# Performance work log

Measured on AMD Instinct MI355X. Metric: run time of the kernel, lower is better.

## Reference

```python
import jax, jax.numpy as jnp
import numpy as np

D_MODEL = 512
N_HEAD = 8


def setup_inputs() -> dict:
    key = jax.random.key(0)
    ks = jax.random.split(key, 9)
    s = 1.0 / np.sqrt(D_MODEL)
    inp = {
        "x": jax.random.normal(ks[0], (2, 4096, D_MODEL), dtype=jnp.float32),
        "wq": jax.random.uniform(ks[1], (D_MODEL, D_MODEL), jnp.float32, -s, s),
        "bq": jax.random.uniform(ks[2], (D_MODEL,), jnp.float32, -s, s),
        "wk": jax.random.uniform(ks[3], (D_MODEL, D_MODEL), jnp.float32, -s, s),
        "bk": jax.random.uniform(ks[4], (D_MODEL,), jnp.float32, -s, s),
        "wv": jax.random.uniform(ks[5], (D_MODEL, D_MODEL), jnp.float32, -s, s),
        "bv": jax.random.uniform(ks[6], (D_MODEL,), jnp.float32, -s, s),
        "wo": jax.random.uniform(ks[7], (D_MODEL, D_MODEL), jnp.float32, -s, s),
        "bo": jax.random.uniform(ks[8], (D_MODEL,), jnp.float32, -s, s),
    }
    return inp


def reference(x, wq, bq, wk, bk, wv, bv, wo, bo):
    B, S, D = x.shape
    H = N_HEAD
    Dh = D // H

    def split_heads(t):  # [B,S,D] -> [B,H,S,Dh]
        return t.reshape(B, S, H, Dh).transpose(0, 2, 1, 3)

    q = split_heads(x @ wq.T + bq)
    k = split_heads(x @ wk.T + bk)
    v = split_heads(x @ wv.T + bv)

    # explicit (unfused) attention, matching the torch module
    score = jnp.einsum("bhsd,bhtd->bhst", q, k) / jnp.sqrt(jnp.float32(Dh))
    attn = jax.nn.softmax(score, axis=-1)
    out = jnp.einsum("bhst,bhtd->bhsd", attn, v)  # [B,H,S,Dh]

    out = out.transpose(0, 2, 1, 3).reshape(B, S, D)
    return out @ wo.T + bo
```

## Files before the change

kernel.cpp:

```cpp
#include <hip/hip_runtime.h>
#include <math.h>

#define S_LEN 4096
#define DMODEL 512
#define NHEAD 8
#define E_ELEMS ((size_t)8192 * 512)
#define QSCALE 0.18033688f

typedef __attribute__((ext_vector_type(8))) short bf16x8;
typedef __attribute__((ext_vector_type(4))) float f32x4;
typedef __attribute__((ext_vector_type(16))) float f32x16;
typedef unsigned short u16;
typedef unsigned int u32;

__device__ __forceinline__ u16 f2bf(float f) {
    u32 u = __float_as_uint(f);
    u += 0x7FFFu + ((u >> 16) & 1u);
    return (u16)(u >> 16);
}

#define MFMA16(a, b, c) __builtin_amdgcn_mfma_f32_16x16x32_bf16((a), (b), (c), 0, 0, 0)
#define MFMA32(a, b, c) __builtin_amdgcn_mfma_f32_32x32x16_bf16((a), (b), (c), 0, 0, 0)

__global__ __launch_bounds__(256) void cvt_x(const float* __restrict__ in,
                                             u16* __restrict__ out, int n4) {
    const int i = blockIdx.x * 256 + threadIdx.x;
    if (i >= n4) return;
    const float4 v = ((const float4*)in)[i];
    uint2 hp;
    hp.x = (u32)f2bf(v.x) | ((u32)f2bf(v.y) << 16);
    hp.y = (u32)f2bf(v.z) | ((u32)f2bf(v.w) << 16);
    ((uint2*)out)[i] = hp;
}

__global__ __launch_bounds__(256) void cvt_w(
    const float* __restrict__ wq, const float* __restrict__ wk,
    const float* __restrict__ wv, const float* __restrict__ wo,
    u16* __restrict__ oq, u16* __restrict__ ok,
    u16* __restrict__ ov, u16* __restrict__ oo) {
    const int i = blockIdx.x * 256 + threadIdx.x;
    {
        const float4 v = ((const float4*)wq)[i];
        uint2 hp;
        hp.x = (u32)f2bf(v.x * QSCALE) | ((u32)f2bf(v.y * QSCALE) << 16);
        hp.y = (u32)f2bf(v.z * QSCALE) | ((u32)f2bf(v.w * QSCALE) << 16);
        ((uint2*)oq)[i] = hp;
    }
    {
        const float4 v = ((const float4*)wk)[i];
        uint2 hp;
        hp.x = (u32)f2bf(v.x) | ((u32)f2bf(v.y) << 16);
        hp.y = (u32)f2bf(v.z) | ((u32)f2bf(v.w) << 16);
        ((uint2*)ok)[i] = hp;
    }
    {
        const float4 v = ((const float4*)wv)[i];
        uint2 hp;
        hp.x = (u32)f2bf(v.x) | ((u32)f2bf(v.y) << 16);
        hp.y = (u32)f2bf(v.z) | ((u32)f2bf(v.w) << 16);
        ((uint2*)ov)[i] = hp;
    }
    {
        const float4 v = ((const float4*)wo)[i];
        uint2 hp;
        hp.x = (u32)f2bf(v.x) | ((u32)f2bf(v.y) << 16);
        hp.y = (u32)f2bf(v.z) | ((u32)f2bf(v.w) << 16);
        ((uint2*)oo)[i] = hp;
    }
}

template<int MODE>
__global__ __launch_bounds__(256) void proj2_kernel(
    const u16* __restrict__ Abf,
    const u16* __restrict__ W0, const float* __restrict__ Bi0,
    const u16* __restrict__ W1, const float* __restrict__ Bi1,
    u16* __restrict__ Qo, u16* __restrict__ Ko, float* __restrict__ Out)
{
    __shared__ __align__(16) u16 sm[16384];
    u16* As = sm;
    u16* Bs = sm + 8192;

    const int tid = threadIdx.x;
    const int w = tid >> 6, l = tid & 63, g = (l >> 4), c = l & 15;
    const int wr = w >> 1, wc = w & 1;
    const int bm = blockIdx.x * 128;
    const int n0 = blockIdx.y * 128;
    const int z = (MODE == 0) ? blockIdx.z : 0;
    const u16* W   = z ? W1 : W0;
    const float* Bi = z ? Bi1 : Bi0;
    const float bsc = (MODE == 0 && z == 0) ? QSCALE : 1.0f;

    const int sr = l >> 3;
    const int slot = l & 7;

    f32x4 acc[4][4];
    #pragma unroll
    for (int i = 0; i < 4; ++i)
        #pragma unroll
        for (int j = 0; j < 4; ++j) acc[i][j] = (f32x4){0.f, 0.f, 0.f, 0.f};

    #pragma unroll 1
    for (int kt = 0; kt < 8; ++kt) {
        const int k0 = kt * 64;
        __syncthreads();
        #pragma unroll
        for (int i = 0; i < 4; ++i) {
            const int row = i * 32 + w * 8 + sr;
            const int scol = (slot ^ (row & 7)) * 8;
            __builtin_amdgcn_global_load_lds(
                Abf + (size_t)(bm + row) * DMODEL + k0 + scol,
                As + (i * 32 + w * 8) * 64, 16, 0, 0);
            __builtin_amdgcn_global_load_lds(
                W + (size_t)(n0 + row) * DMODEL + k0 + scol,
                Bs + (i * 32 + w * 8) * 64, 16, 0, 0);
        }
        __syncthreads();

        #pragma unroll
        for (int kc = 0; kc < 2; ++kc) {
            bf16x8 a[4], b[4];
            #pragma unroll
            for (int mf = 0; mf < 4; ++mf) {
                const int ra = wr * 64 + mf * 16 + c;
                a[mf] = *(const bf16x8*)(As + ra * 64 + (((kc * 4 + g) ^ (ra & 7)) * 8));
            }
            #pragma unroll
            for (int nf = 0; nf < 4; ++nf) {
                const int rb = wc * 64 + nf * 16 + c;
                b[nf] = *(const bf16x8*)(Bs + rb * 64 + (((kc * 4 + g) ^ (rb & 7)) * 8));
            }
            #pragma unroll
            for (int mf = 0; mf < 4; ++mf)
                #pragma unroll
                for (int nf = 0; nf < 4; ++nf)
                    acc[mf][nf] = MFMA16(a[mf], b[nf], acc[mf][nf]);
        }
    }

    #pragma unroll
    for (int mf = 0; mf < 4; ++mf)
        #pragma unroll
        for (int nf = 0; nf < 4; ++nf) {
            const int n = n0 + wc * 64 + nf * 16 + c;
            const float bias = Bi[n] * bsc;
            #pragma unroll
            for (int r = 0; r < 4; ++r) {
                const int m = bm + wr * 64 + mf * 16 + 4 * g + r;
                const float v = acc[mf][nf][r] + bias;
                if (MODE == 1) {
                    Out[(size_t)m * DMODEL + n] = v;
                } else {
                    const int b = m >> 12, s = m & (S_LEN - 1);
                    const int hh = n >> 6, dd = n & 63;
                    const size_t o = ((size_t)((b * NHEAD + hh) * S_LEN + s)) * 64 + dd;
                    if (z == 0) Qo[o] = f2bf(v);
                    else        Ko[o] = f2bf(v);
                }
            }
        }
}

__global__ __launch_bounds__(256) void proj_v_kernel(
    const u16* __restrict__ Abf, const u16* __restrict__ Wv,
    const float* __restrict__ Bv, u16* __restrict__ Vt)
{
    __shared__ __align__(16) u16 sm[18432];
    u16* Ah = sm;
    u16* Bh = sm + 9216;

    const int tid = threadIdx.x;
    const int w = tid >> 6, lane = tid & 63, g = lane >> 4, c = lane & 15;
    const int bm = blockIdx.x * 128;
    const int n0 = blockIdx.y * 64;

    f32x4 acc[2][4];
    #pragma unroll
    for (int a = 0; a < 2; ++a)
        #pragma unroll
        for (int b = 0; b < 4; ++b) acc[a][b] = (f32x4){0.f, 0.f, 0.f, 0.f};

    #pragma unroll 1
    for (int kt = 0; kt < 8; ++kt) {
        const int k0 = kt * 64;
        __syncthreads();
        #pragma unroll
        for (int i = 0; i < 4; ++i) {
            const int slot = i * 256 + tid;
            const int r = slot >> 3, c8 = slot & 7;
            *(uint4*)(Ah + r * 72 + c8 * 8) =
                *(const uint4*)(Abf + (size_t)(bm + r) * DMODEL + k0 + c8 * 8);
        }
        #pragma unroll
        for (int i = 0; i < 2; ++i) {
            const int slot = i * 256 + tid;
            const int r = slot >> 3, c8 = slot & 7;
            *(uint4*)(Bh + r * 72 + c8 * 8) =
                *(const uint4*)(Wv + (size_t)(n0 + r) * DMODEL + k0 + c8 * 8);
        }
        __syncthreads();

        #pragma unroll
        for (int kc = 0; kc < 2; ++kc) {
            bf16x8 a[2], b[4];
            #pragma unroll
            for (int mf = 0; mf < 2; ++mf)
                a[mf] = *(const bf16x8*)(Ah + (w * 32 + mf * 16 + c) * 72 + kc * 32 + g * 8);
            #pragma unroll
            for (int nf = 0; nf < 4; ++nf)
                b[nf] = *(const bf16x8*)(Bh + (nf * 16 + c) * 72 + kc * 32 + g * 8);
            #pragma unroll
            for (int mf = 0; mf < 2; ++mf)
                #pragma unroll
                for (int nf = 0; nf < 4; ++nf)
                    acc[mf][nf] = MFMA16(a[mf], b[nf], acc[mf][nf]);
        }
    }

    __syncthreads();
    float* scr = (float*)sm;
    #pragma unroll
    for (int mf = 0; mf < 2; ++mf)
        #pragma unroll
        for (int nf = 0; nf < 4; ++nf) {
            const float bias = Bv[n0 + nf * 16 + c];
            #pragma unroll
            for (int r = 0; r < 4; ++r)
                scr[(w * 32 + mf * 16 + 4 * g + r) * 72 + nf * 16 + c] =
                    acc[mf][nf][r] + bias;
        }
    __syncthreads();
    const int d = tid & 63, sb = tid >> 6;
    const int b = bm >> 12, h = n0 >> 6;
    const size_t obase =
        ((size_t)((b * NHEAD + h) * 64 + d)) * S_LEN + (bm & (S_LEN - 1)) + sb * 32;
    u16 th[32];
    #pragma unroll
    for (int j = 0; j < 32; ++j)
        th[j] = f2bf(scr[(sb * 32 + j) * 72 + d]);
    #pragma unroll
    for (int q = 0; q < 4; ++q)
        *(uint4*)(Vt + obase + q * 8) = *(const uint4*)&th[q * 8];
}

__global__ __launch_bounds__(512, 4) void attn_kernel(
    const u16* __restrict__ Qb, const u16* __restrict__ Kb,
    const u16* __restrict__ Vt, u16* __restrict__ AO)
{
    __shared__ __align__(16) u16 sm[32768];

    const int tid = threadIdx.x;
    const int w = tid >> 6, l = tid & 63;
    const int kvg = w >> 2, wq = w & 3;
    const int r0 = l & 31, hi = l >> 5;

    const int f = blockIdx.x;
    const int wg = (f & 7) * 64 + (f >> 3);
    const int bh = wg >> 5, qb = wg & 31;
    const int b = bh >> 3, h = bh & 7;

    const size_t hoff = (size_t)bh * S_LEN * 64;
    const int qw = qb * 128 + wq * 32;
    const int kv0 = kvg * 2048;

    bf16x8 qf[4];
    #pragma unroll
    for (int kc = 0; kc < 4; ++kc)
        qf[kc] = *(const bf16x8*)(Qb + hoff + (size_t)(qw + r0) * 64 + kc * 16 + hi * 8);

    const int rbase = r0 * 64;
    int soff[4];
    #pragma unroll
    for (int j = 0; j < 4; ++j) soff[j] = ((2 * j + hi) ^ (r0 & 7)) * 8;

    const int srow0 = wq * 16 + (l >> 3);
    const int slot  = l & 7;
    const int srow1 = srow0 + 8;
    const u16* srcK0 = Kb + hoff + (size_t)(kv0 + srow0) * 64 + ((slot ^ (srow0 & 7)) * 8);
    const u16* srcK1 = Kb + hoff + (size_t)(kv0 + srow1) * 64 + ((slot ^ (srow1 & 7)) * 8);
    const u16* srcV0 = Vt + ((size_t)bh * 64 + srow0) * S_LEN + kv0 + ((slot ^ (srow0 & 7)) * 8);
    const u16* srcV1 = Vt + ((size_t)bh * 64 + srow1) * S_LEN + kv0 + ((slot ^ (srow1 & 7)) * 8);

    u16* const grp = sm + kvg * 16384;

#define STAGE(bufb, t) do {                                                        \
        u16* kb_ = grp + (bufb) * 8192 + wq * 1024;                                \
        u16* vb_ = kb_ + 4096;                                                     \
        __builtin_amdgcn_global_load_lds(srcK0 + (size_t)(t) * 4096, kb_,       16, 0, 0); \
        __builtin_amdgcn_global_load_lds(srcK1 + (size_t)(t) * 4096, kb_ + 512, 16, 0, 0); \
        __builtin_amdgcn_global_load_lds(srcV0 + (size_t)(t) * 64,   vb_,       16, 0, 0); \
        __builtin_amdgcn_global_load_lds(srcV1 + (size_t)(t) * 64,   vb_ + 512, 16, 0, 0); \
    } while (0)

    f32x16 o0 = {0.f,0.f,0.f,0.f,0.f,0.f,0.f,0.f,0.f,0.f,0.f,0.f,0.f,0.f,0.f,0.f};
    f32x16 o1 = {0.f,0.f,0.f,0.f,0.f,0.f,0.f,0.f,0.f,0.f,0.f,0.f,0.f,0.f,0.f,0.f};
    f32x16 lacc = {0.f,0.f,0.f,0.f,0.f,0.f,0.f,0.f,0.f,0.f,0.f,0.f,0.f,0.f,0.f,0.f};

    STAGE(0, 0);
    __syncthreads();
    int buf = 0;

    #pragma unroll 1
    for (int t = 0; t < 32; ++t) {
        if (t + 1 < 32) STAGE(buf ^ 1, t + 1);

        const u16* Kb_s = grp + buf * 8192;
        const u16* Vb_s = Kb_s + 4096;

        f32x16 s0 = {0.f,0.f,0.f,0.f,0.f,0.f,0.f,0.f,0.f,0.f,0.f,0.f,0.f,0.f,0.f,0.f};
        f32x16 s1 = {0.f,0.f,0.f,0.f,0.f,0.f,0.f,0.f,0.f,0.f,0.f,0.f,0.f,0.f,0.f,0.f};
        __builtin_amdgcn_s_setprio(1);
        #pragma unroll
        for (int kc = 0; kc < 4; ++kc) {
            const bf16x8 k0 = *(const bf16x8*)(Kb_s + rbase + soff[kc]);
            const bf16x8 k1 = *(const bf16x8*)(Kb_s + 2048 + rbase + soff[kc]);
            s0 = MFMA32(k0, qf[kc], s0);
            s1 = MFMA32(k1, qf[kc], s1);
        }
        __builtin_amdgcn_s_setprio(0);

        bf16x8 pa[4];
        #pragma unroll
        for (int kvf = 0; kvf < 2; ++kvf) {
            f32x16 pex;
            #pragma unroll
            for (int r = 0; r < 16; ++r)
                pex[r] = __builtin_amdgcn_exp2f(kvf ? s1[r] : s0[r]);
            lacc += pex;
            #pragma unroll
            for (int hf = 0; hf < 2; ++hf) {
                const int rb = hf * 8;
                u32 x0, y0, x1, y1;
                asm("v_cvt_pk_bf16_f32 %0, %1, %2" : "=v"(x0) : "v"(pex[rb+0]), "v"(pex[rb+1]));
                asm("v_cvt_pk_bf16_f32 %0, %1, %2" : "=v"(y0) : "v"(pex[rb+4]), "v"(pex[rb+5]));
                asm("v_cvt_pk_bf16_f32 %0, %1, %2" : "=v"(x1) : "v"(pex[rb+2]), "v"(pex[rb+3]));
                asm("v_cvt_pk_bf16_f32 %0, %1, %2" : "=v"(y1) : "v"(pex[rb+6]), "v"(pex[rb+7]));
                asm volatile("v_permlane32_swap_b32 %0, %1" : "+v"(x0), "+v"(y0));
                asm volatile("v_permlane32_swap_b32 %0, %1" : "+v"(x1), "+v"(y1));
                union { u32 u[4]; bf16x8 v; } P;
                P.u[0] = x0; P.u[1] = x1; P.u[2] = y0; P.u[3] = y1;
                pa[kvf * 2 + hf] = P.v;
            }
        }

        __builtin_amdgcn_s_setprio(1);
        #pragma unroll
        for (int kvc = 0; kvc < 4; ++kvc) {
            const bf16x8 v0 = *(const bf16x8*)(Vb_s + rbase + soff[kvc]);
            const bf16x8 v1 = *(const bf16x8*)(Vb_s + 2048 + rbase + soff[kvc]);
            o0 = MFMA32(pa[kvc], v0, o0);
            o1 = MFMA32(pa[kvc], v1, o1);
        }
        __builtin_amdgcn_s_setprio(0);

        __syncthreads();
        buf ^= 1;
    }
#undef STAGE

    float lsum = 0.f;
    #pragma unroll
    for (int r = 0; r < 16; ++r) lsum += lacc[r];
    lsum += __shfl_xor(lsum, 32);

    float* scrF = (float*)sm;
    float* Lsh  = scrF + 8192;
    if (hi == 0) Lsh[w * 32 + r0] = lsum;
    if (kvg == 1) {
        #pragma unroll
        for (int r = 0; r < 16; ++r) {
            const int q = (r & 3) + 8 * (r >> 2) + 4 * hi;
            scrF[wq * 2048 + q * 64 + r0]      = o0[r];
            scrF[wq * 2048 + q * 64 + 32 + r0] = o1[r];
        }
    }
    __syncthreads();
    if (kvg == 0) {
        #pragma unroll
        for (int r = 0; r < 16; ++r) {
            const int q = (r & 3) + 8 * (r >> 2) + 4 * hi;
            const float L = Lsh[wq * 32 + q] + Lsh[(wq + 4) * 32 + q];
            const float inv = 1.0f / L;
            const int s = qw + q;
            const size_t base = ((size_t)b * S_LEN + s) * DMODEL + h * 64;
            AO[base + r0]      = f2bf((o0[r] + scrF[wq * 2048 + q * 64 + r0])      * inv);
            AO[base + 32 + r0] = f2bf((o1[r] + scrF[wq * 2048 + q * 64 + 32 + r0]) * inv);
        }
    }
}

extern "C" void kernel_launch(void* const* d_in, const int* in_sizes, int n_in,
                              void* d_out, int out_size, void* d_ws, size_t ws_size,
                              hipStream_t stream)
{
    const float* x  = (const float*)d_in[0];
    const float* wq = (const float*)d_in[1];
    const float* bq = (const float*)d_in[2];
    const float* wk = (const float*)d_in[3];
    const float* bk = (const float*)d_in[4];
    const float* wv = (const float*)d_in[5];
    const float* bv = (const float*)d_in[6];
    const float* wo = (const float*)d_in[7];
    const float* bo = (const float*)d_in[8];

    u16* ws = (u16*)d_ws;
    const size_t E = E_ELEMS;
    u16* xbf  = ws;
    u16* Qbf  = ws + E;
    u16* Kbf  = ws + 2 * E;
    u16* Vtbf = ws + 3 * E;
    u16* wqbf = ws + 4 * E;
    u16* wkbf = wqbf + DMODEL * DMODEL;
    u16* wvbf = wkbf + DMODEL * DMODEL;
    u16* wobf = wvbf + DMODEL * DMODEL;

    cvt_x<<<dim3(4096), 256, 0, stream>>>(x, xbf, (int)(E / 4));
    cvt_w<<<dim3(256), 256, 0, stream>>>(wq, wk, wv, wo, wqbf, wkbf, wvbf, wobf);

    proj2_kernel<0><<<dim3(64, 4, 2), 256, 0, stream>>>(
        xbf, wqbf, bq, wkbf, bk, Qbf, Kbf, nullptr);

    proj_v_kernel<<<dim3(64, 8), 256, 0, stream>>>(xbf, wvbf, bv, Vtbf);

    attn_kernel<<<dim3(512), 512, 0, stream>>>(Qbf, Kbf, Vtbf, xbf);

    proj2_kernel<1><<<dim3(64, 4), 256, 0, stream>>>(
        xbf, wobf, bo, nullptr, nullptr, nullptr, nullptr, (float*)d_out);
}
```

Before: 143.0 us.

## Split attention KV range across four blocks and combine partials in separate kernel

Attention blocks drop from 512 threads with two intra-block KV groups to 256 threads each handling one quarter of the KV sequence, which quadruples the grid to 2048 blocks. Each block writes unnormalized bf16 partial outputs and row sums to workspace, and a new combine kernel adds the four partials and normalizes. The intent is better occupancy and load balance across CUs. The cost is an extra launch, extra global traffic for four partial output tensors, and added rounding from storing the partials in bf16.

```diff
diff --git a/kernel.cpp b/kernel.cpp
--- a/kernel.cpp
+++ b/kernel.cpp
@@ -17,6 +17,9 @@
     u32 u = __float_as_uint(f);
     u += 0x7FFFu + ((u >> 16) & 1u);
     return (u16)(u >> 16);
+}
+__device__ __forceinline__ float bf2f(u16 h) {
+    return __uint_as_float((u32)h << 16);
 }
 
 #define MFMA16(a, b, c) __builtin_amdgcn_mfma_f32_16x16x32_bf16((a), (b), (c), 0, 0, 0)
@@ -242,25 +245,24 @@
         *(uint4*)(Vt + obase + q * 8) = *(const uint4*)&th[q * 8];
 }
 
-__global__ __launch_bounds__(512, 4) void attn_kernel(
+__global__ __launch_bounds__(256, 4) void attn_kernel(
     const u16* __restrict__ Qb, const u16* __restrict__ Kb,
-    const u16* __restrict__ Vt, u16* __restrict__ AO)
+    const u16* __restrict__ Vt, u16* __restrict__ OpB, float* __restrict__ Lp)
 {
-    __shared__ __align__(16) u16 sm[32768];
+    __shared__ __align__(16) u16 sm[16384];
 
     const int tid = threadIdx.x;
     const int w = tid >> 6, l = tid & 63;
-    const int kvg = w >> 2, wq = w & 3;
     const int r0 = l & 31, hi = l >> 5;
 
     const int f = blockIdx.x;
-    const int wg = (f & 7) * 64 + (f >> 3);
-    const int bh = wg >> 5, qb = wg & 31;
+    const int wg = (f & 7) * 256 + (f >> 3);
+    const int bh = wg >> 7, kvq = (wg >> 5) & 3, qb = wg & 31;
     const int b = bh >> 3, h = bh & 7;
 
     const size_t hoff = (size_t)bh * S_LEN * 64;
-    const int qw = qb * 128 + wq * 32;
-    const int kv0 = kvg * 2048;
+    const int qw = qb * 128 + w * 32;
+    const int kv0 = kvq * 1024;
 
     bf16x8 qf[4];
     #pragma unroll
@@ -272,7 +274,7 @@
     #pragma unroll
     for (int j = 0; j < 4; ++j) soff[j] = ((2 * j + hi) ^ (r0 & 7)) * 8;
 
-    const int srow0 = wq * 16 + (l >> 3);
+    const int srow0 = w * 16 + (l >> 3);
     const int slot  = l & 7;
     const int srow1 = srow0 + 8;
     const u16* srcK0 = Kb + hoff + (size_t)(kv0 + srow0) * 64 + ((slot ^ (srow0 & 7)) * 8);
@@ -280,10 +282,8 @@
     const u16* srcV0 = Vt + ((size_t)bh * 64 + srow0) * S_LEN + kv0 + ((slot ^ (srow0 & 7)) * 8);
     const u16* srcV1 = Vt + ((size_t)bh * 64 + srow1) * S_LEN + kv0 + ((slot ^ (srow1 & 7)) * 8);
 
-    u16* const grp = sm + kvg * 16384;
-
 #define STAGE(bufb, t) do {                                                        \
-        u16* kb_ = grp + (bufb) * 8192 + wq * 1024;                                \
+        u16* kb_ = sm + (bufb) * 8192 + w * 1024;                                  \
         u16* vb_ = kb_ + 4096;                                                     \
         __builtin_amdgcn_global_load_lds(srcK0 + (size_t)(t) * 4096, kb_,       16, 0, 0); \
         __builtin_amdgcn_global_load_lds(srcK1 + (size_t)(t) * 4096, kb_ + 512, 16, 0, 0); \
@@ -300,10 +300,10 @@
     int buf = 0;
 
     #pragma unroll 1
-    for (int t = 0; t < 32; ++t) {
-        if (t + 1 < 32) STAGE(buf ^ 1, t + 1);
-
-        const u16* Kb_s = grp + buf * 8192;
+    for (int t = 0; t < 16; ++t) {
+        if (t + 1 < 16) STAGE(buf ^ 1, t + 1);
+
+        const u16* Kb_s = sm + buf * 8192;
         const u16* Vb_s = Kb_s + 4096;
 
         f32x16 s0 = {0.f,0.f,0.f,0.f,0.f,0.f,0.f,0.f,0.f,0.f,0.f,0.f,0.f,0.f,0.f,0.f};
@@ -361,31 +361,48 @@
     #pragma unroll
     for (int r = 0; r < 16; ++r) lsum += lacc[r];
     lsum += __shfl_xor(lsum, 32);
-
-    float* scrF = (float*)sm;
-    float* Lsh  = scrF + 8192;
-    if (hi == 0) Lsh[w * 32 + r0] = lsum;
-    if (kvg == 1) {
+    if (hi == 0)
+        Lp[((size_t)kvq * 16 + bh) * S_LEN + qw + r0] = lsum;
+
+    u16* Ob = OpB + (size_t)kvq * E_ELEMS + (size_t)b * S_LEN * DMODEL;
+    #pragma unroll
+    for (int df = 0; df < 2; ++df) {
         #pragma unroll
         for (int r = 0; r < 16; ++r) {
+            const float ov = df ? o1[r] : o0[r];
             const int q = (r & 3) + 8 * (r >> 2) + 4 * hi;
-            scrF[wq * 2048 + q * 64 + r0]      = o0[r];
-            scrF[wq * 2048 + q * 64 + 32 + r0] = o1[r];
-        }
-    }
-    __syncthreads();
-    if (kvg == 0) {
-        #pragma unroll
-        for (int r = 0; r < 16; ++r) {
-            const int q = (r & 3) + 8 * (r >> 2) + 4 * hi;
-            const float L = Lsh[wq * 32 + q] + Lsh[(wq + 4) * 32 + q];
-            const float inv = 1.0f / L;
-            const int s = qw + q;
-            const size_t base = ((size_t)b * S_LEN + s) * DMODEL + h * 64;
-            AO[base + r0]      = f2bf((o0[r] + scrF[wq * 2048 + q * 64 + r0])      * inv);
-            AO[base + 32 + r0] = f2bf((o1[r] + scrF[wq * 2048 + q * 64 + 32 + r0]) * inv);
-        }
-    }
+            Ob[(size_t)(qw + q) * DMODEL + h * 64 + df * 32 + r0] = f2bf(ov);
+        }
+    }
+}
+
+__global__ __launch_bounds__(256) void combine_kernel(
+    const u16* __restrict__ Op, const float* __restrict__ Lp,
+    u16* __restrict__ A)
+{
+    const int i = blockIdx.x * 256 + threadIdx.x;
+    const int m = i >> 6;
+    const int col = (i & 63) * 8;
+    const int b = m >> 12, s = m & (S_LEN - 1), h = col >> 6;
+
+    float lt = 0.f;
+    #pragma unroll
+    for (int kq = 0; kq < 4; ++kq)
+        lt += Lp[((size_t)kq * 16 + b * 8 + h) * S_LEN + s];
+    const float inv = 1.0f / lt;
+
+    float acc[8] = {};
+    #pragma unroll
+    for (int kq = 0; kq < 4; ++kq) {
+        const uint4 v = *(const uint4*)(Op + (size_t)kq * E_ELEMS + (size_t)m * DMODEL + col);
+        const u16* p = (const u16*)&v;
+        #pragma unroll
+        for (int j = 0; j < 8; ++j) acc[j] += bf2f(p[j]);
+    }
+    u16 r[8];
+    #pragma unroll
+    for (int j = 0; j < 8; ++j) r[j] = f2bf(acc[j] * inv);
+    *(uint4*)(A + (size_t)m * DMODEL + col) = *(const uint4*)r;
 }
 
 extern "C" void kernel_launch(void* const* d_in, const int* in_sizes, int n_in,
@@ -412,6 +429,8 @@
     u16* wkbf = wqbf + DMODEL * DMODEL;
     u16* wvbf = wkbf + DMODEL * DMODEL;
     u16* wobf = wvbf + DMODEL * DMODEL;
+    u16* OpB  = wobf + DMODEL * DMODEL;
+    float* Lp = (float*)(OpB + 4 * E);
 
     cvt_x<<<dim3(4096), 256, 0, stream>>>(x, xbf, (int)(E / 4));
     cvt_w<<<dim3(256), 256, 0, stream>>>(wq, wk, wv, wo, wqbf, wkbf, wvbf, wobf);
@@ -421,7 +440,9 @@
 
     proj_v_kernel<<<dim3(64, 8), 256, 0, stream>>>(xbf, wvbf, bv, Vtbf);
 
-    attn_kernel<<<dim3(512), 512, 0, stream>>>(Qbf, Kbf, Vtbf, xbf);
+    attn_kernel<<<dim3(2048), 256, 0, stream>>>(Qbf, Kbf, Vtbf, OpB, Lp);
+
+    combine_kernel<<<dim3(2048), 256, 0, stream>>>(OpB, Lp, xbf);
 
     proj2_kernel<1><<<dim3(64, 4), 256, 0, stream>>>(
         xbf, wobf, bo, nullptr, nullptr, nullptr, nullptr, (float*)d_out);
```

Result: slower. 148.8 us (+4.1%).
